# Kernel tuning notes

Hardware: AMD Instinct MI355X
Metric: run time of the kernel (lower is better)

The kernel has to match this reference:

```python
import jax, jax.numpy as jnp
import numpy as np

act = jax.nn.softplus

def _lin(h, W, b):
    return h @ W + b

def _residual_stack(h, Ws, bs):
    # Ws: [L,2,D,D], bs: [L,2,D]; Residual: x + Lin(act(Lin(act(x))))
    for i in range(Ws.shape[0]):
        t = _lin(act(h), Ws[i, 0], bs[i, 0])
        t = _lin(act(t), Ws[i, 1], bs[i, 1])
        h = t + h
    return h

def setup_inputs() -> dict:
    key = jax.random.key(0)
    N, E, D, R = 40000, 640000, 128, 64
    n_int, n_atomic, n_out = 2, 2, 1
    ks = jax.random.split(key, 24)
    s = 1.0 / np.sqrt(D)
    sr = 1.0 / np.sqrt(R)
    inp = {
        'x': jax.random.normal(ks[0], (N, D), jnp.float32),
        'g_ij': jax.random.uniform(ks[1], (E, R), jnp.float32),
        'idx_i': jax.random.randint(ks[2], (E,), 0, N, jnp.int32),
        'idx_j': jax.random.randint(ks[3], (E,), 0, N, jnp.int32),
        'n_atoms': N,
        'u': jax.random.uniform(ks[4], (D,), jnp.float32),  # torch.rand(n_atom_basis)
        'W_g': jax.random.normal(ks[5], (R, D), jnp.float32) * sr,
        'b_g': jnp.zeros((D,), jnp.float32),
        'W_j': jax.random.normal(ks[6], (D, D), jnp.float32) * s,
        'b_j': jnp.zeros((D,), jnp.float32),
        'W_i': jax.random.normal(ks[7], (D, D), jnp.float32) * s,
        'b_i': jnp.zeros((D,), jnp.float32),
        'W_f': jax.random.normal(ks[8], (D, D), jnp.float32) * s,
        'b_f': jnp.zeros((D,), jnp.float32),
        'Wres_int': jax.random.normal(ks[9], (n_int, 2, D, D), jnp.float32) * s,
        'bres_int': jnp.zeros((n_int, 2, D), jnp.float32),
        'Wres_atom': jax.random.normal(ks[10], (n_atomic, 2, D, D), jnp.float32) * s,
        'bres_atom': jnp.zeros((n_atomic, 2, D), jnp.float32),
        'Wres_out': jax.random.normal(ks[11], (n_out, 2, D, D), jnp.float32) * s,
        'bres_out': jnp.zeros((n_out, 2, D), jnp.float32),
        'W_out': jax.random.normal(ks[12], (D, D), jnp.float32) * s,
        'b_out': jnp.zeros((D,), jnp.float32),
    }
    return inp

def reference(x, g_ij, idx_i, idx_j, n_atoms, u,
              W_g, b_g, W_j, b_j, W_i, b_i, W_f, b_f,
              Wres_int, bres_int, Wres_atom, bres_atom,
              Wres_out, bres_out, W_out, b_out):
    # --- PhysNetInteraction ---
    x_j = x[idx_j]                                   # [E,D] gather
    xp = u * x                                       # random feature scale
    vp = act(_lin(act(x_j), W_j, b_j)) * _lin(g_ij, W_g, b_g)   # [E,D]
    vm = act(_lin(act(x), W_i, b_i))                 # [N,D]
    v = jax.ops.segment_sum(vp, idx_i, num_segments=n_atoms) + vm
    v = _residual_stack(v, Wres_int, bres_int)
    v = act(v)
    h = xp + _lin(v, W_f, b_f)
    # --- atomic residuals ---
    h = _residual_stack(h, Wres_atom, bres_atom)
    # --- Output block ---
    o = _residual_stack(h, Wres_out, bres_out)
    o = _lin(act(o), W_out, b_out)
    return (o, h)
```

## Files before the change

kernel.cpp:

```cpp
#include <hip/hip_runtime.h>


#define D 128
#define TILE 64
#define TILE2 128
#define LDP 136
#define SLOT 16384
#define EPB 64

typedef __attribute__((ext_vector_type(8))) short s8v;
typedef __attribute__((ext_vector_type(4))) unsigned short us4;
typedef __attribute__((ext_vector_type(4))) float f32x4;

struct Frag { f32x4 v[8]; };
struct WReg { s8v w[4]; };

__device__ __forceinline__ float sp_act(float x) {
    float t = __builtin_amdgcn_exp2f(-fabsf(x) * 1.44269504088896f);
    return fmaxf(x, 0.f) + 0.69314718055994f * __builtin_amdgcn_logf(1.0f + t);
}
__device__ __forceinline__ unsigned short f2bf(float f) {
    unsigned int u = __float_as_uint(f);
    u += 0x7fffu + ((u >> 16) & 1u);
    return (unsigned short)(u >> 16);
}
__device__ __forceinline__ float bf2f(unsigned short h) {
    return __uint_as_float(((unsigned int)h) << 16);
}

__global__ void prep_weights(
    const float* __restrict__ Wj, const float* __restrict__ Wi,
    const float* __restrict__ Wf, const float* __restrict__ Wout,
    const float* __restrict__ Wri, const float* __restrict__ Wra,
    const float* __restrict__ Wro, const float* __restrict__ Wg,
    unsigned short* __restrict__ wt)
{
    int id = blockIdx.x;
    const float* src;
    int K = D;
    if      (id == 0)  src = Wj;
    else if (id == 1)  src = Wi;
    else if (id == 2)  src = Wf;
    else if (id == 3)  src = Wout;
    else if (id < 8)   src = Wri + (id - 4) * D * D;
    else if (id < 12)  src = Wra + (id - 8) * D * D;
    else if (id < 14)  src = Wro + (id - 12) * D * D;
    else             { src = Wg; K = 64; }
    unsigned short* dst = wt + id * SLOT;
    int total = K * D;
    for (int e = threadIdx.x; e < total; e += blockDim.x) {
        int k = e >> 7, n = e & 127;
        dst[n * K + k] = f2bf(src[e]);
    }
}

template <int NT>
__device__ __forceinline__ void load_w128(const unsigned short* __restrict__ wt,
                                          unsigned short (*Wl)[LDP], int t) {
#pragma unroll
    for (int q = 0; q < 2048 / NT; ++q) {
        int c = t + q * NT;
        int row = c >> 4;
        int k = (c & 15) * 8;
        *(s8v*)&Wl[row][k] = *(const s8v*)(wt + row * 128 + k);
    }
}

__device__ __forceinline__ void mm128(const unsigned short (*Ax)[LDP],
                                      const unsigned short (*Wl)[LDP],
                                      int wrow, int lane, Frag& acc) {
    int r = lane & 15, g4 = lane >> 4;
#pragma unroll
    for (int k0 = 0; k0 < 4; ++k0) {
        s8v a = *(const s8v*)&Ax[wrow + r][k0 * 32 + g4 * 8];
#pragma unroll
        for (int n = 0; n < 8; ++n) {
            s8v b = *(const s8v*)&Wl[n * 16 + r][k0 * 32 + g4 * 8];
            acc.v[n] = __builtin_amdgcn_mfma_f32_16x16x32_bf16(a, b, acc.v[n], 0, 0, 0);
        }
    }
}

__global__ __launch_bounds__(256) void node_pre(
    const float* __restrict__ x, const unsigned short* __restrict__ wt,
    const float* __restrict__ bj, const float* __restrict__ bi,
    unsigned short* __restrict__ P, float* __restrict__ v, int N)
{
    __shared__ __align__(16) unsigned short Ax[TILE][LDP];
    __shared__ __align__(16) unsigned short Wl[D][LDP];
    int t = threadIdx.x;
    int r0 = blockIdx.x * TILE;
#pragma unroll
    for (int q = 0; q < 8; ++q) {
        int c = t + q * 256;
        int row = c >> 5;
        int col = (c & 31) * 4;
        int gr = r0 + row;
        f32x4 xv = {0.f, 0.f, 0.f, 0.f};
        if (gr < N) xv = *(const f32x4*)(x + (size_t)gr * D + col);
        us4 w = { f2bf(sp_act(xv[0])), f2bf(sp_act(xv[1])),
                  f2bf(sp_act(xv[2])), f2bf(sp_act(xv[3])) };
        *(us4*)&Ax[row][col] = w;
    }
    load_w128<256>(wt + 0 * SLOT, Wl, t);
    s8v wreg0, wreg1, wreg2, wreg3, wreg4, wreg5, wreg6, wreg7;
    {
        const unsigned short* wsrc = wt + 1 * SLOT;
        int row = t >> 4, k = (t & 15) * 8;
        wreg0 = *(const s8v*)(wsrc + (row +   0) * 128 + k);
        wreg1 = *(const s8v*)(wsrc + (row +  16) * 128 + k);
        wreg2 = *(const s8v*)(wsrc + (row +  32) * 128 + k);
        wreg3 = *(const s8v*)(wsrc + (row +  48) * 128 + k);
        wreg4 = *(const s8v*)(wsrc + (row +  64) * 128 + k);
        wreg5 = *(const s8v*)(wsrc + (row +  80) * 128 + k);
        wreg6 = *(const s8v*)(wsrc + (row +  96) * 128 + k);
        wreg7 = *(const s8v*)(wsrc + (row + 112) * 128 + k);
    }
    __syncthreads();

    int lane = t & 63, wv = t >> 6, wrow = wv * 16;
    int r = lane & 15, g4 = lane >> 4;
    Frag acc;
#pragma unroll
    for (int n = 0; n < 8; ++n) { float b = bj[n * 16 + r]; acc.v[n] = (f32x4){b, b, b, b}; }
    mm128(Ax, Wl, wrow, lane, acc);
#pragma unroll
    for (int i = 0; i < 4; ++i) {
        int row = r0 + wrow + g4 * 4 + i;
        if (row < N) {
            s8v p;
#pragma unroll
            for (int n = 0; n < 8; ++n) p[n] = (short)f2bf(sp_act(acc.v[n][i]));
            __builtin_nontemporal_store(p, (s8v*)(P + (size_t)row * D + r * 8));
        }
    }
    __syncthreads();
    {
        int row = t >> 4, k = (t & 15) * 8;
        *(s8v*)&Wl[row +   0][k] = wreg0;
        *(s8v*)&Wl[row +  16][k] = wreg1;
        *(s8v*)&Wl[row +  32][k] = wreg2;
        *(s8v*)&Wl[row +  48][k] = wreg3;
        *(s8v*)&Wl[row +  64][k] = wreg4;
        *(s8v*)&Wl[row +  80][k] = wreg5;
        *(s8v*)&Wl[row +  96][k] = wreg6;
        *(s8v*)&Wl[row + 112][k] = wreg7;
    }
    __syncthreads();
#pragma unroll
    for (int n = 0; n < 8; ++n) { float b = bi[n * 16 + r]; acc.v[n] = (f32x4){b, b, b, b}; }
    mm128(Ax, Wl, wrow, lane, acc);
#pragma unroll
    for (int i = 0; i < 4; ++i) {
        int row = r0 + wrow + g4 * 4 + i;
        if (row < N) {
            f32x4 lo, hi;
#pragma unroll
            for (int n = 0; n < 4; ++n) {
                lo[n] = sp_act(acc.v[n][i]);
                hi[n] = sp_act(acc.v[n + 4][i]);
            }
            __builtin_nontemporal_store(lo, (f32x4*)(v + (size_t)row * D + r * 8));
            __builtin_nontemporal_store(hi, (f32x4*)(v + (size_t)row * D + r * 8 + 4));
        }
    }
}

__global__ void zero_ints(int* __restrict__ a, int n) {
    int i = blockIdx.x * blockDim.x + threadIdx.x;
    if (i < n) a[i] = 0;
}
__global__ void hist_kernel(const int* __restrict__ idx_i, int* __restrict__ counts, int E) {
    for (int e = blockIdx.x * blockDim.x + threadIdx.x; e < E; e += gridDim.x * blockDim.x)
        atomicAdd(&counts[idx_i[e]], 1);
}
__global__ __launch_bounds__(1024) void scan_kernel(const int* __restrict__ counts,
                                                    int* __restrict__ offsets, int n) {
    __shared__ int wsum[16];
    int t = threadIdx.x, lane = t & 63, w = t >> 6;
    int carry = 0;
    for (int base = 0; base < n; base += 1024) {
        int i = base + t;
        int val = (i < n) ? counts[i] : 0;
        int s = val;
#pragma unroll
        for (int d = 1; d < 64; d <<= 1) {
            int y = __shfl_up(s, d, 64);
            if (lane >= d) s += y;
        }
        if (lane == 63) wsum[w] = s;
        __syncthreads();
        if (w == 0) {
            int ws = (lane < 16) ? wsum[lane] : 0;
#pragma unroll
            for (int d = 1; d < 16; d <<= 1) {
                int y = __shfl_up(ws, d, 64);
                if (lane >= d) ws += y;
            }
            if (lane < 16) wsum[lane] = ws;
        }
        __syncthreads();
        int wpre = (w == 0) ? 0 : wsum[w - 1];
        if (i < n) offsets[i] = carry + wpre + (s - val);
        int total = wsum[15];
        __syncthreads();
        carry += total;
    }
}
__global__ void scatter_kernel(const int* __restrict__ idx_i,
                               const int* __restrict__ idx_j,
                               const int* __restrict__ offsets,
                               int* __restrict__ cursor, int* __restrict__ perm,
                               int* __restrict__ sni, int* __restrict__ snj, int E) {
    for (int e = blockIdx.x * blockDim.x + threadIdx.x; e < E; e += gridDim.x * blockDim.x) {
        int i = idx_i[e];
        int p = offsets[i] + atomicAdd(&cursor[i], 1);
        perm[p] = e;
        sni[p] = i;
        snj[p] = idx_j[e];
    }
}

__global__ __launch_bounds__(256) void edge_gather(
    const float* __restrict__ g, const int* __restrict__ spe,
    const int* __restrict__ sni, const int* __restrict__ snj,
    const unsigned short* __restrict__ wtg, const float* __restrict__ bg,
    const unsigned short* __restrict__ P, float* __restrict__ v, int E)
{
    __shared__ __align__(16) unsigned char smem[33792];
    __shared__ int s_ni[EPB];
    unsigned short (*Gx)[72] = (unsigned short(*)[72])smem;
    unsigned short (*WG)[72] = (unsigned short(*)[72])(smem + 9216);
    float (*Vx)[132] = (float(*)[132])smem;

    int t = threadIdx.x;
    int e0 = blockIdx.x * EPB;
    int lane = t & 63, wv = t >> 6;
    int r = lane & 15, g4 = lane >> 4;

    if (t < EPB) {
        int e = e0 + t;
        s_ni[t] = (e < E) ? sni[e] : -1;
    }

    int pe0, pe1, pe2, pe3;
    {
        int brow = t >> 4;
        pe0 = (e0 + brow +  0 < E) ? spe[e0 + brow +  0] : -1;
        pe1 = (e0 + brow + 16 < E) ? spe[e0 + brow + 16] : -1;
        pe2 = (e0 + brow + 32 < E) ? spe[e0 + brow + 32] : -1;
        pe3 = (e0 + brow + 48 < E) ? spe[e0 + brow + 48] : -1;
    }
    {
        int col = (t & 15) * 4;
        f32x4 gv0 = {0.f,0.f,0.f,0.f}, gv1 = {0.f,0.f,0.f,0.f};
        f32x4 gv2 = {0.f,0.f,0.f,0.f}, gv3 = {0.f,0.f,0.f,0.f};
        if (pe0 >= 0) gv0 = __builtin_nontemporal_load((const f32x4*)(g + (size_t)pe0 * 64 + col));
        if (pe1 >= 0) gv1 = __builtin_nontemporal_load((const f32x4*)(g + (size_t)pe1 * 64 + col));
        if (pe2 >= 0) gv2 = __builtin_nontemporal_load((const f32x4*)(g + (size_t)pe2 * 64 + col));
        if (pe3 >= 0) gv3 = __builtin_nontemporal_load((const f32x4*)(g + (size_t)pe3 * 64 + col));
        int brow = t >> 4;
        us4 w0 = { f2bf(gv0[0]), f2bf(gv0[1]), f2bf(gv0[2]), f2bf(gv0[3]) };
        us4 w1 = { f2bf(gv1[0]), f2bf(gv1[1]), f2bf(gv1[2]), f2bf(gv1[3]) };
        us4 w2 = { f2bf(gv2[0]), f2bf(gv2[1]), f2bf(gv2[2]), f2bf(gv2[3]) };
        us4 w3 = { f2bf(gv3[0]), f2bf(gv3[1]), f2bf(gv3[2]), f2bf(gv3[3]) };
        *(us4*)&Gx[brow +  0][col] = w0;
        *(us4*)&Gx[brow + 16][col] = w1;
        *(us4*)&Gx[brow + 32][col] = w2;
        *(us4*)&Gx[brow + 48][col] = w3;
    }
#pragma unroll
    for (int q = 0; q < 4; ++q) {
        int c = t + q * 256;
        int row = c >> 3;
        int k = (c & 7) * 8;
        *(s8v*)&WG[row][k] = *(const s8v*)(wtg + row * 64 + k);
    }
    s8v pv0, pv1, pv2, pv3;
    {
        int eb = e0 + wv * 16 + g4 * 4;
        int nj0 = (eb + 0 < E) ? snj[eb + 0] : 0;
        int nj1 = (eb + 1 < E) ? snj[eb + 1] : 0;
        int nj2 = (eb + 2 < E) ? snj[eb + 2] : 0;
        int nj3 = (eb + 3 < E) ? snj[eb + 3] : 0;
        pv0 = *(const s8v*)(P + (size_t)nj0 * D + r * 8);
        pv1 = *(const s8v*)(P + (size_t)nj1 * D + r * 8);
        pv2 = *(const s8v*)(P + (size_t)nj2 * D + r * 8);
        pv3 = *(const s8v*)(P + (size_t)nj3 * D + r * 8);
    }
    __syncthreads();

    Frag acc;
#pragma unroll
    for (int n = 0; n < 8; ++n) { float b = bg[n * 16 + r]; acc.v[n] = (f32x4){b, b, b, b}; }
#pragma unroll
    for (int k0 = 0; k0 < 2; ++k0) {
        s8v a = *(const s8v*)&Gx[wv * 16 + r][k0 * 32 + g4 * 8];
#pragma unroll
        for (int n = 0; n < 8; ++n) {
            s8v b = *(const s8v*)&WG[n * 16 + r][k0 * 32 + g4 * 8];
            acc.v[n] = __builtin_amdgcn_mfma_f32_16x16x32_bf16(a, b, acc.v[n], 0, 0, 0);
        }
    }
    __syncthreads();

#pragma unroll
    for (int i = 0; i < 4; ++i) {
        int el = wv * 16 + g4 * 4 + i;
        bool valid = (e0 + el) < E;
        s8v pvv = (i == 0) ? pv0 : (i == 1) ? pv1 : (i == 2) ? pv2 : pv3;
        f32x4 lo, hi;
#pragma unroll
        for (int n = 0; n < 4; ++n) {
            lo[n] = valid ? acc.v[n][i]     * bf2f((unsigned short)pvv[n])     : 0.f;
            hi[n] = valid ? acc.v[n + 4][i] * bf2f((unsigned short)pvv[n + 4]) : 0.f;
        }
        *(f32x4*)&Vx[el][r * 8]     = lo;
        *(f32x4*)&Vx[el][r * 8 + 4] = hi;
    }
    __syncthreads();

    int f = t & 127, half = t >> 7;
    int estart = half * 32;
    int ecap = E - e0; if (ecap > EPB) ecap = EPB;
    int eend = estart + 32; if (eend > ecap) eend = ecap;
    if (estart < eend) {
        float accv = 0.f;
        int cur = s_ni[estart];
        for (int e = estart; e < eend; ++e) {
            int node = s_ni[e];
            if (node != cur) {
                unsafeAtomicAdd(v + (size_t)cur * D + f, accv);
                accv = 0.f; cur = node;
            }
            accv += Vx[e][f];
        }
        unsafeAtomicAdd(v + (size_t)cur * D + f, accv);
    }
}

__device__ __forceinline__ void stage_w(WReg& wr,
                                        const unsigned short* __restrict__ wtp, int t) {
#pragma unroll
    for (int q = 0; q < 4; ++q) {
        int c = t + q * 512; int row = c >> 4; int k = (c & 15) * 8;
        wr.w[q] = *(const s8v*)(wtp + row * 128 + k);
    }
}

template <bool RESID>
__device__ __forceinline__ Frag do_layer(
    const Frag in, const Frag resid,
    const float* __restrict__ bias,
    WReg& wreg, const unsigned short* __restrict__ next_wt,
    unsigned short (*Ax)[LDP], unsigned short (*Wl)[LDP],
    int t, int lane, int wrow, int r, int g4)
{
    __syncthreads();
#pragma unroll
    for (int n = 0; n < 8; ++n)
#pragma unroll
        for (int i = 0; i < 4; ++i)
            Ax[wrow + g4 * 4 + i][n * 16 + r] = f2bf(sp_act(in.v[n][i]));
#pragma unroll
    for (int q = 0; q < 4; ++q) {
        int c = t + q * 512; int row = c >> 4; int k = (c & 15) * 8;
        *(s8v*)&Wl[row][k] = wreg.w[q];
    }
    if (next_wt) stage_w(wreg, next_wt, t);
    __syncthreads();
    Frag out;
#pragma unroll
    for (int n = 0; n < 8; ++n) {
        float b = bias[n * 16 + r];
        f32x4 bb = {b, b, b, b};
        out.v[n] = RESID ? bb + resid.v[n] : bb;
    }
    mm128(Ax, Wl, wrow, lane, out);
    return out;
}

__device__ __forceinline__ void store_tile(
    const Frag val, float* __restrict__ dst, int r0, int N,
    float (*St)[132], int t, int wv, int r, int g4)
{
#pragma unroll
    for (int half = 0; half < 2; ++half) {
        __syncthreads();
        if ((wv >> 2) == half) {
            int lr = (wv & 3) * 16 + g4 * 4;
#pragma unroll
            for (int n = 0; n < 8; ++n)
#pragma unroll
                for (int i = 0; i < 4; ++i)
                    St[lr + i][n * 16 + r] = val.v[n][i];
        }
        __syncthreads();
#pragma unroll
        for (int q = 0; q < 4; ++q) {
            int idx = t + q * 512;
            int row = idx >> 5, c4 = (idx & 31) * 4;
            int gr = r0 + half * 64 + row;
            if (gr < N) {
                f32x4 vv = *(const f32x4*)&St[row][c4];
                __builtin_nontemporal_store(vv, (f32x4*)(dst + (size_t)gr * D + c4));
            }
        }
    }
}

__global__ __launch_bounds__(512) void phaseB(
    const float* __restrict__ vin, const float* __restrict__ x,
    const float* __restrict__ u, const unsigned short* __restrict__ wt,
    const float* __restrict__ bri, const float* __restrict__ bra,
    const float* __restrict__ bro, const float* __restrict__ bfv,
    const float* __restrict__ bout,
    float* __restrict__ o_out, float* __restrict__ h_out, int N)
{
    __shared__ __align__(16) unsigned short Ax[TILE2][LDP];
    __shared__ __align__(16) unsigned short Wl[D][LDP];
    float (*St)[132] = (float(*)[132])Wl;
    int t = threadIdx.x, lane = t & 63, wv = t >> 6, wrow = wv * 16;
    int r = lane & 15, g4 = lane >> 4;
    int r0 = blockIdx.x * TILE2;

    WReg wreg;
    stage_w(wreg, wt + 4 * SLOT, t);

    Frag h;
#pragma unroll
    for (int i = 0; i < 4; ++i) {
        int row = r0 + wrow + g4 * 4 + i;
        f32x4 lo = {0.f, 0.f, 0.f, 0.f}, hi = {0.f, 0.f, 0.f, 0.f};
        if (row < N) {
            lo = __builtin_nontemporal_load((const f32x4*)(vin + (size_t)row * D + r * 8));
            hi = __builtin_nontemporal_load((const f32x4*)(vin + (size_t)row * D + r * 8 + 4));
        }
#pragma unroll
        for (int n = 0; n < 4; ++n) { h.v[n][i] = lo[n]; h.v[n + 4][i] = hi[n]; }
    }

    Frag t0;
    t0 = do_layer<false>(h,  h, bri + 0 * D, wreg, wt +  5 * SLOT, Ax, Wl, t, lane, wrow, r, g4);
    h  = do_layer<true >(t0, h, bri + 1 * D, wreg, wt +  6 * SLOT, Ax, Wl, t, lane, wrow, r, g4);
    t0 = do_layer<false>(h,  h, bri + 2 * D, wreg, wt +  7 * SLOT, Ax, Wl, t, lane, wrow, r, g4);
    h  = do_layer<true >(t0, h, bri + 3 * D, wreg, wt +  2 * SLOT, Ax, Wl, t, lane, wrow, r, g4);
    Frag ux;
#pragma unroll
    for (int n = 0; n < 8; ++n)
#pragma unroll
        for (int i = 0; i < 4; ++i) {
            int row = r0 + wrow + g4 * 4 + i;
            float xv = (row < N) ? x[(size_t)row * D + n * 16 + r] : 0.f;
            ux.v[n][i] = u[n * 16 + r] * xv;
        }
    h  = do_layer<true >(h,  ux, bfv, wreg, wt + 8 * SLOT, Ax, Wl, t, lane, wrow, r, g4);
    t0 = do_layer<false>(h,  h, bra + 0 * D, wreg, wt +  9 * SLOT, Ax, Wl, t, lane, wrow, r, g4);
    h  = do_layer<true >(t0, h, bra + 1 * D, wreg, wt + 10 * SLOT, Ax, Wl, t, lane, wrow, r, g4);
    t0 = do_layer<false>(h,  h, bra + 2 * D, wreg, wt + 11 * SLOT, Ax, Wl, t, lane, wrow, r, g4);
    h  = do_layer<true >(t0, h, bra + 3 * D, wreg, wt + 12 * SLOT, Ax, Wl, t, lane, wrow, r, g4);
    store_tile(h, h_out, r0, N, St, t, wv, r, g4);
    t0 = do_layer<false>(h,  h, bro + 0 * D, wreg, wt + 13 * SLOT, Ax, Wl, t, lane, wrow, r, g4);
    h  = do_layer<true >(t0, h, bro + 1 * D, wreg, wt +  3 * SLOT, Ax, Wl, t, lane, wrow, r, g4);
    t0 = do_layer<false>(h,  h, bout,        wreg, nullptr,        Ax, Wl, t, lane, wrow, r, g4);
    store_tile(t0, o_out, r0, N, St, t, wv, r, g4);
}

extern "C" void kernel_launch(void* const* d_in, const int* in_sizes, int n_in,
                              void* d_out, int out_size, void* d_ws, size_t ws_size,
                              hipStream_t stream)
{
    const float* x     = (const float*)d_in[0];
    const float* g     = (const float*)d_in[1];
    const int*   idx_i = (const int*)d_in[2];
    const int*   idx_j = (const int*)d_in[3];
    const float* u     = (const float*)d_in[5];
    const float* Wg    = (const float*)d_in[6];
    const float* bg    = (const float*)d_in[7];
    const float* Wj    = (const float*)d_in[8];
    const float* bj    = (const float*)d_in[9];
    const float* Wi    = (const float*)d_in[10];
    const float* bi    = (const float*)d_in[11];
    const float* Wf    = (const float*)d_in[12];
    const float* bf    = (const float*)d_in[13];
    const float* Wri   = (const float*)d_in[14];
    const float* bri   = (const float*)d_in[15];
    const float* Wra   = (const float*)d_in[16];
    const float* bra   = (const float*)d_in[17];
    const float* Wro   = (const float*)d_in[18];
    const float* bro   = (const float*)d_in[19];
    const float* Wout  = (const float*)d_in[20];
    const float* bout  = (const float*)d_in[21];

    int N = in_sizes[0] / D;
    int E = in_sizes[2];

    float* out = (float*)d_out;
    float* v     = out;
    float* h_out = out + (size_t)N * D;
    unsigned short* P = (unsigned short*)h_out;
    unsigned short* wt = (unsigned short*)d_ws;

    int* ibase   = (int*)(out + (size_t)N * D + (size_t)N * D / 2);
    int* counts  = ibase;
    int* offsets = ibase + N;
    int* cursor  = ibase + 2 * (size_t)N;
    int* perm    = ibase + 3 * (size_t)N;
    int* sni     = perm + E;
    int* snj     = sni + E;

    prep_weights<<<15, 256, 0, stream>>>(Wj, Wi, Wf, Wout, Wri, Wra, Wro, Wg, wt);

    int nb = (N + TILE - 1) / TILE;
    node_pre<<<nb, 256, 0, stream>>>(x, wt, bj, bi, P, v, N);

    zero_ints<<<(3 * N + 255) / 256, 256, 0, stream>>>(ibase, 3 * N);
    hist_kernel<<<1024, 256, 0, stream>>>(idx_i, counts, E);
    scan_kernel<<<1, 1024, 0, stream>>>(counts, offsets, N);
    scatter_kernel<<<1024, 256, 0, stream>>>(idx_i, idx_j, offsets, cursor,
                                             perm, sni, snj, E);

    int eb = (E + EPB - 1) / EPB;
    edge_gather<<<eb, 256, 0, stream>>>(g, perm, sni, snj, wt + 14 * SLOT, bg,
                                        P, v, E);

    int nb2 = (N + TILE2 - 1) / TILE2;
    phaseB<<<nb2, 512, 0, stream>>>(v, x, u, wt, bri, bra, bro, bf, bout,
                                    out, h_out, N);
}
```

Measured before the change: 321.2 us.

## Fuse zeroing and histogram into earlier kernels, shrink phaseB tile, bf16 edge staging

Measured after the change: 295.9 us. 7.9% less time.

```diff
diff --git a/kernel.cpp b/kernel.cpp
--- a/kernel.cpp
+++ b/kernel.cpp
@@ -3,7 +3,6 @@
 
 #define D 128
 #define TILE 64
-#define TILE2 128
 #define LDP 136
 #define SLOT 16384
 #define EPB 64
@@ -13,7 +12,7 @@
 typedef __attribute__((ext_vector_type(4))) float f32x4;
 
 struct Frag { f32x4 v[8]; };
-struct WReg { s8v w[4]; };
+struct WReg8 { s8v w[8]; };
 
 __device__ __forceinline__ float sp_act(float x) {
     float t = __builtin_amdgcn_exp2f(-fabsf(x) * 1.44269504088896f);
@@ -33,9 +32,14 @@
     const float* __restrict__ Wf, const float* __restrict__ Wout,
     const float* __restrict__ Wri, const float* __restrict__ Wra,
     const float* __restrict__ Wro, const float* __restrict__ Wg,
-    unsigned short* __restrict__ wt)
+    unsigned short* __restrict__ wt, int* __restrict__ zbase, int zn)
 {
     int id = blockIdx.x;
+    if (id >= 15) {
+        int i = (id - 15) * 256 + threadIdx.x;
+        if (i < zn) zbase[i] = 0;
+        return;
+    }
     const float* src;
     int K = D;
     if      (id == 0)  src = Wj;
@@ -54,12 +58,11 @@
     }
 }
 
-template <int NT>
 __device__ __forceinline__ void load_w128(const unsigned short* __restrict__ wt,
                                           unsigned short (*Wl)[LDP], int t) {
 #pragma unroll
-    for (int q = 0; q < 2048 / NT; ++q) {
-        int c = t + q * NT;
+    for (int q = 0; q < 8; ++q) {
+        int c = t + q * 256;
         int row = c >> 4;
         int k = (c & 15) * 8;
         *(s8v*)&Wl[row][k] = *(const s8v*)(wt + row * 128 + k);
@@ -84,7 +87,8 @@
 __global__ __launch_bounds__(256) void node_pre(
     const float* __restrict__ x, const unsigned short* __restrict__ wt,
     const float* __restrict__ bj, const float* __restrict__ bi,
-    unsigned short* __restrict__ P, float* __restrict__ v, int N)
+    unsigned short* __restrict__ P, float* __restrict__ v,
+    const int* __restrict__ idx_i, int* __restrict__ counts, int E, int N)
 {
     __shared__ __align__(16) unsigned short Ax[TILE][LDP];
     __shared__ __align__(16) unsigned short Wl[D][LDP];
@@ -102,19 +106,12 @@
                   f2bf(sp_act(xv[2])), f2bf(sp_act(xv[3])) };
         *(us4*)&Ax[row][col] = w;
     }
-    load_w128<256>(wt + 0 * SLOT, Wl, t);
-    s8v wreg0, wreg1, wreg2, wreg3, wreg4, wreg5, wreg6, wreg7;
-    {
-        const unsigned short* wsrc = wt + 1 * SLOT;
-        int row = t >> 4, k = (t & 15) * 8;
-        wreg0 = *(const s8v*)(wsrc + (row +   0) * 128 + k);
-        wreg1 = *(const s8v*)(wsrc + (row +  16) * 128 + k);
-        wreg2 = *(const s8v*)(wsrc + (row +  32) * 128 + k);
-        wreg3 = *(const s8v*)(wsrc + (row +  48) * 128 + k);
-        wreg4 = *(const s8v*)(wsrc + (row +  64) * 128 + k);
-        wreg5 = *(const s8v*)(wsrc + (row +  80) * 128 + k);
-        wreg6 = *(const s8v*)(wsrc + (row +  96) * 128 + k);
-        wreg7 = *(const s8v*)(wsrc + (row + 112) * 128 + k);
+    load_w128(wt + 0 * SLOT, Wl, t);
+    WReg8 wr;
+#pragma unroll
+    for (int q = 0; q < 8; ++q) {
+        int c = t + q * 256; int row = c >> 4; int k = (c & 15) * 8;
+        wr.w[q] = *(const s8v*)(wt + 1 * SLOT + row * 128 + k);
     }
     __syncthreads();
 
@@ -135,16 +132,10 @@
         }
     }
     __syncthreads();
-    {
-        int row = t >> 4, k = (t & 15) * 8;
-        *(s8v*)&Wl[row +   0][k] = wreg0;
-        *(s8v*)&Wl[row +  16][k] = wreg1;
-        *(s8v*)&Wl[row +  32][k] = wreg2;
-        *(s8v*)&Wl[row +  48][k] = wreg3;
-        *(s8v*)&Wl[row +  64][k] = wreg4;
-        *(s8v*)&Wl[row +  80][k] = wreg5;
-        *(s8v*)&Wl[row +  96][k] = wreg6;
-        *(s8v*)&Wl[row + 112][k] = wreg7;
+#pragma unroll
+    for (int q = 0; q < 8; ++q) {
+        int c = t + q * 256; int row = c >> 4; int k = (c & 15) * 8;
+        *(s8v*)&Wl[row][k] = wr.w[q];
     }
     __syncthreads();
 #pragma unroll
@@ -164,16 +155,10 @@
             __builtin_nontemporal_store(hi, (f32x4*)(v + (size_t)row * D + r * 8 + 4));
         }
     }
-}
-
-__global__ void zero_ints(int* __restrict__ a, int n) {
-    int i = blockIdx.x * blockDim.x + threadIdx.x;
-    if (i < n) a[i] = 0;
-}
-__global__ void hist_kernel(const int* __restrict__ idx_i, int* __restrict__ counts, int E) {
-    for (int e = blockIdx.x * blockDim.x + threadIdx.x; e < E; e += gridDim.x * blockDim.x)
+    for (int e = blockIdx.x * blockDim.x + t; e < E; e += gridDim.x * blockDim.x)
         atomicAdd(&counts[idx_i[e]], 1);
 }
+
 __global__ __launch_bounds__(1024) void scan_kernel(const int* __restrict__ counts,
                                                     int* __restrict__ offsets, int n) {
     __shared__ int wsum[16];
@@ -227,11 +212,11 @@
     const unsigned short* __restrict__ wtg, const float* __restrict__ bg,
     const unsigned short* __restrict__ P, float* __restrict__ v, int E)
 {
-    __shared__ __align__(16) unsigned char smem[33792];
+    __shared__ __align__(16) unsigned char smem[27648];
     __shared__ int s_ni[EPB];
     unsigned short (*Gx)[72] = (unsigned short(*)[72])smem;
     unsigned short (*WG)[72] = (unsigned short(*)[72])(smem + 9216);
-    float (*Vx)[132] = (float(*)[132])smem;
+    unsigned short (*Vx)[136] = (unsigned short(*)[136])smem;
 
     int t = threadIdx.x;
     int e0 = blockIdx.x * EPB;
@@ -309,14 +294,13 @@
         int el = wv * 16 + g4 * 4 + i;
         bool valid = (e0 + el) < E;
         s8v pvv = (i == 0) ? pv0 : (i == 1) ? pv1 : (i == 2) ? pv2 : pv3;
-        f32x4 lo, hi;
-#pragma unroll
-        for (int n = 0; n < 4; ++n) {
-            lo[n] = valid ? acc.v[n][i]     * bf2f((unsigned short)pvv[n])     : 0.f;
-            hi[n] = valid ? acc.v[n + 4][i] * bf2f((unsigned short)pvv[n + 4]) : 0.f;
-        }
-        *(f32x4*)&Vx[el][r * 8]     = lo;
-        *(f32x4*)&Vx[el][r * 8 + 4] = hi;
+        s8v outv;
+#pragma unroll
+        for (int n = 0; n < 8; ++n) {
+            float val = valid ? acc.v[n][i] * bf2f((unsigned short)pvv[n]) : 0.f;
+            outv[n] = (short)f2bf(val);
+        }
+        *(s8v*)&Vx[el][r * 8] = outv;
     }
     __syncthreads();
 
@@ -333,17 +317,17 @@
                 unsafeAtomicAdd(v + (size_t)cur * D + f, accv);
                 accv = 0.f; cur = node;
             }
-            accv += Vx[e][f];
+            accv += bf2f(Vx[e][f]);
         }
         unsafeAtomicAdd(v + (size_t)cur * D + f, accv);
     }
 }
 
-__device__ __forceinline__ void stage_w(WReg& wr,
+__device__ __forceinline__ void stage_w(WReg8& wr,
                                         const unsigned short* __restrict__ wtp, int t) {
 #pragma unroll
-    for (int q = 0; q < 4; ++q) {
-        int c = t + q * 512; int row = c >> 4; int k = (c & 15) * 8;
+    for (int q = 0; q < 8; ++q) {
+        int c = t + q * 256; int row = c >> 4; int k = (c & 15) * 8;
         wr.w[q] = *(const s8v*)(wtp + row * 128 + k);
     }
 }
@@ -352,7 +336,7 @@
 __device__ __forceinline__ Frag do_layer(
     const Frag in, const Frag resid,
     const float* __restrict__ bias,
-    WReg& wreg, const unsigned short* __restrict__ next_wt,
+    WReg8& wreg, const unsigned short* __restrict__ next_wt,
     unsigned short (*Ax)[LDP], unsigned short (*Wl)[LDP],
     int t, int lane, int wrow, int r, int g4)
 {
@@ -363,8 +347,8 @@
         for (int i = 0; i < 4; ++i)
             Ax[wrow + g4 * 4 + i][n * 16 + r] = f2bf(sp_act(in.v[n][i]));
 #pragma unroll
-    for (int q = 0; q < 4; ++q) {
-        int c = t + q * 512; int row = c >> 4; int k = (c & 15) * 8;
+    for (int q = 0; q < 8; ++q) {
+        int c = t + q * 256; int row = c >> 4; int k = (c & 15) * 8;
         *(s8v*)&Wl[row][k] = wreg.w[q];
     }
     if (next_wt) stage_w(wreg, next_wt, t);
@@ -384,32 +368,27 @@
     const Frag val, float* __restrict__ dst, int r0, int N,
     float (*St)[132], int t, int wv, int r, int g4)
 {
-#pragma unroll
-    for (int half = 0; half < 2; ++half) {
-        __syncthreads();
-        if ((wv >> 2) == half) {
-            int lr = (wv & 3) * 16 + g4 * 4;
-#pragma unroll
-            for (int n = 0; n < 8; ++n)
-#pragma unroll
-                for (int i = 0; i < 4; ++i)
-                    St[lr + i][n * 16 + r] = val.v[n][i];
-        }
-        __syncthreads();
-#pragma unroll
-        for (int q = 0; q < 4; ++q) {
-            int idx = t + q * 512;
-            int row = idx >> 5, c4 = (idx & 31) * 4;
-            int gr = r0 + half * 64 + row;
-            if (gr < N) {
-                f32x4 vv = *(const f32x4*)&St[row][c4];
-                __builtin_nontemporal_store(vv, (f32x4*)(dst + (size_t)gr * D + c4));
-            }
-        }
-    }
-}
-
-__global__ __launch_bounds__(512) void phaseB(
+    int wrow = wv * 16;
+    __syncthreads();
+#pragma unroll
+    for (int n = 0; n < 8; ++n)
+#pragma unroll
+        for (int i = 0; i < 4; ++i)
+            St[wrow + g4 * 4 + i][n * 16 + r] = val.v[n][i];
+    __syncthreads();
+#pragma unroll
+    for (int q = 0; q < 8; ++q) {
+        int idx = t + q * 256;
+        int row = idx >> 5, c4 = (idx & 31) * 4;
+        int gr = r0 + row;
+        if (gr < N) {
+            f32x4 vv = *(const f32x4*)&St[row][c4];
+            __builtin_nontemporal_store(vv, (f32x4*)(dst + (size_t)gr * D + c4));
+        }
+    }
+}
+
+__global__ __launch_bounds__(256) void phaseB(
     const float* __restrict__ vin, const float* __restrict__ x,
     const float* __restrict__ u, const unsigned short* __restrict__ wt,
     const float* __restrict__ bri, const float* __restrict__ bra,
@@ -417,14 +396,14 @@
     const float* __restrict__ bout,
     float* __restrict__ o_out, float* __restrict__ h_out, int N)
 {
-    __shared__ __align__(16) unsigned short Ax[TILE2][LDP];
+    __shared__ __align__(16) unsigned short Ax[TILE][LDP];
     __shared__ __align__(16) unsigned short Wl[D][LDP];
     float (*St)[132] = (float(*)[132])Wl;
     int t = threadIdx.x, lane = t & 63, wv = t >> 6, wrow = wv * 16;
     int r = lane & 15, g4 = lane >> 4;
-    int r0 = blockIdx.x * TILE2;
-
-    WReg wreg;
+    int r0 = blockIdx.x * TILE;
+
+    WReg8 wreg;
     stage_w(wreg, wt + 4 * SLOT, t);
 
     Frag h;
@@ -509,13 +488,13 @@
     int* sni     = perm + E;
     int* snj     = sni + E;
 
-    prep_weights<<<15, 256, 0, stream>>>(Wj, Wi, Wf, Wout, Wri, Wra, Wro, Wg, wt);
+    int zn = 3 * N;
+    prep_weights<<<15 + (zn + 255) / 256, 256, 0, stream>>>(
+        Wj, Wi, Wf, Wout, Wri, Wra, Wro, Wg, wt, ibase, zn);
 
     int nb = (N + TILE - 1) / TILE;
-    node_pre<<<nb, 256, 0, stream>>>(x, wt, bj, bi, P, v, N);
-
-    zero_ints<<<(3 * N + 255) / 256, 256, 0, stream>>>(ibase, 3 * N);
-    hist_kernel<<<1024, 256, 0, stream>>>(idx_i, counts, E);
+    node_pre<<<nb, 256, 0, stream>>>(x, wt, bj, bi, P, v, idx_i, counts, E, N);
+
     scan_kernel<<<1, 1024, 0, stream>>>(counts, offsets, N);
     scatter_kernel<<<1024, 256, 0, stream>>>(idx_i, idx_j, offsets, cursor,
                                              perm, sni, snj, E);
@@ -524,7 +503,6 @@
     edge_gather<<<eb, 256, 0, stream>>>(g, perm, sni, snj, wt + 14 * SLOT, bg,
                                         P, v, E);
 
-    int nb2 = (N + TILE2 - 1) / TILE2;
-    phaseB<<<nb2, 512, 0, stream>>>(v, x, u, wt, bri, bra, bro, bf, bout,
-                                    out, h_out, N);
-}
+    phaseB<<<nb, 256, 0, stream>>>(v, x, u, wt, bri, bra, bro, bf, bout,
+                                   out, h_out, N);
+}
```
